# Optimization experiments

Measured on AMD Instinct MI355X. Metric: run time of the kernel, lower is better.

The kernel has to match this reference:

```python
import jax, jax.numpy as jnp
import numpy as np

B, T, H, HW = 16, 32, 512, 32  # batch, timesteps, hidden channels, spatial size


def setup_inputs() -> dict:
    key = jax.random.key(0)
    k1, k2, k3, k4, k5 = jax.random.split(key, 5)
    x = jax.random.normal(k1, (B, T, HW, HW), dtype=jnp.float32)
    # cell conv: 1x1, (1 + H) -> 4H, with bias (k=1 default, padding 'same')
    W_conv = jax.random.normal(k2, (4 * H, 1 + H, 1, 1), dtype=jnp.float32) * 0.02
    b_conv = jax.random.normal(k3, (4 * H,), dtype=jnp.float32) * 0.02
    # post conv: 3x3, H -> 1, padding 'same'
    W_post = jax.random.normal(k4, (1, H, 3, 3), dtype=jnp.float32) * 0.02
    b_post = jax.random.normal(k5, (1,), dtype=jnp.float32) * 0.02
    return {"x": x, "W_conv": W_conv, "b_conv": b_conv, "W_post": W_post, "b_post": b_post}


def _post_conv(h, W_post, b_post):
    # NCHW 3x3 'same' conv
    y = jax.lax.conv_general_dilated(
        h, W_post, window_strides=(1, 1), padding="SAME",
        dimension_numbers=("NCHW", "OIHW", "NCHW"))
    return y + b_post[None, :, None, None]


def reference(x, W_conv, b_conv, W_post, b_post):
    Wc = W_conv[:, :, 0, 0]  # [4H, 1+H] -- 1x1 conv is a channel GEMM

    def step(carry, xt):
        h, c = carry  # [B,H,32,32] each; xt [B,1,32,32]
        z = jnp.concatenate([xt, h], axis=1)  # [B,1+H,32,32]
        gates = jnp.einsum("bchw,oc->bohw", z, Wc) + b_conv[None, :, None, None]
        i, f, o, g = jnp.split(gates, 4, axis=1)
        # Faithful to source (non-standard gating):
        c = jax.nn.sigmoid(f) * c + jax.nn.sigmoid(i) + jnp.tanh(g)
        h = jax.nn.sigmoid(o) + jnp.tanh(c)
        y = _post_conv(h, W_post, b_post)  # [B,1,32,32]
        return (h, c), y

    h0 = jnp.zeros((x.shape[0], H, HW, HW), dtype=x.dtype)
    c0 = jnp.zeros_like(h0)
    xs = x[:, :, None, :, :].transpose(1, 0, 2, 3, 4)  # [T,B,1,32,32]
    _, ys = jax.lax.scan(step, (h0, c0), xs)  # ys [T,B,1,32,32]
    out = ys[:, :, 0].transpose(1, 0, 2, 3)  # [B,T,32,32] == cat along dim=1
    return out
```

## Files before the change

kernel.cpp:

```cpp
#include <hip/hip_runtime.h>
#include <cstdint>
#include <cstddef>

#define B_    16
#define T_    32
#define H_    512
#define P_    1024
#define NPOS  16384
#define NG    2048

typedef __attribute__((ext_vector_type(8))) short short8;
typedef __attribute__((ext_vector_type(4))) float f32x4;

__device__ __forceinline__ unsigned short f2bf(float f) {
  uint32_t u = __float_as_uint(f);
  u += 0x7fffu + ((u >> 16) & 1u);
  return (unsigned short)(u >> 16);
}
__device__ __forceinline__ float bflo(uint32_t u) { return __uint_as_float(u << 16); }
__device__ __forceinline__ float bfhi(uint32_t u) { return __uint_as_float(u & 0xffff0000u); }

__device__ __forceinline__ float sigf(float x) {
  return __builtin_amdgcn_rcpf(1.0f + __expf(-x));
}
__device__ __forceinline__ float tanhf_(float x) {
  return 1.0f - 2.0f * __builtin_amdgcn_rcpf(__expf(2.0f * x) + 1.0f);
}

__device__ __forceinline__ void gload_lds16(const void* g, void* l) {
  __builtin_amdgcn_global_load_lds(
      (const __attribute__((address_space(1))) void*)g,
      (__attribute__((address_space(3))) void*)l, 16, 0, 0);
}

__global__ void repack_w(const float* __restrict__ Wc, const float* __restrict__ bconv,
                         unsigned short* __restrict__ Wp, float* __restrict__ w0x,
                         float* __restrict__ bx) {
  int idx = blockIdx.x * 256 + threadIdx.x;
  int r = idx >> 9, k = idx & 511;
  int ch = r >> 2, g = r & 3;
  int o = g * 512 + ch;
  Wp[idx] = f2bf(Wc[o * 513 + 1 + k]);
  if (k == 0) { w0x[r] = Wc[o * 513]; bx[r] = bconv[o]; }
}

__global__ void repack_wpost(const float* __restrict__ Wpost, float* __restrict__ wpp) {
  int idx = blockIdx.x * 256 + threadIdx.x;
  if (idx >= 9 * 512) return;
  int j = idx >> 9, c = idx & 511;
  wpp[idx] = Wpost[c * 9 + j];
}

__global__ __launch_bounds__(256, 2)
void lstm_step(const unsigned short* __restrict__ Wp,
               const unsigned short* __restrict__ hprev,
               unsigned short* __restrict__ hnext,
               _Float16* __restrict__ Cst,
               const float* __restrict__ w0x, const float* __restrict__ bxv,
               const float* __restrict__ xin, int t) {
  __shared__ unsigned short As[256 * 64];
  __shared__ unsigned short Bs[128 * 64];

  const int tid = threadIdx.x;
  const int lane = tid & 63;
  const int wv = tid >> 6;
  const int wm = wv >> 1, wn = wv & 1;
  const int q = lane >> 4, l = lane & 15;

  const int lid = blockIdx.x;
  const int xcd = lid & 7;
  const int s   = lid >> 3;
  const int ny  = xcd * 16 + (s & 15);
  const int rx  = s >> 4;
  const int r0  = rx * 256;
  const int n0  = ny * 128;
  const int ch0 = rx * 64;

  const int srow = tid >> 3;
  const int lchunk = (tid & 7) ^ (srow & 7);
  const unsigned short* gA = Wp    + (size_t)(r0 + srow) * 512 + lchunk * 8;
  const unsigned short* gB = hprev + (size_t)(n0 + srow) * 512 + lchunk * 8;
  char* lA = (char*)As + wv * 1024;
  char* lB = (char*)Bs + wv * 1024;

  f32x4 acc[8][4] = {};

  for (int kc = 0; kc < 512; kc += 64) {
#pragma unroll
    for (int j = 0; j < 8; ++j)
      gload_lds16(gA + (size_t)j * (32 * 512) + kc, lA + j * 4096);
#pragma unroll
    for (int j = 0; j < 4; ++j)
      gload_lds16(gB + (size_t)j * (32 * 512) + kc, lB + j * 4096);
    __syncthreads();

#pragma unroll
    for (int kk = 0; kk < 2; ++kk) {
      short8 af[8], bf_[4];
#pragma unroll
      for (int mi = 0; mi < 8; ++mi) {
        int row = wm * 128 + mi * 16 + l;
        int sidx = row * 64 + (((kk * 4 + q) ^ (row & 7)) * 8);
        af[mi] = *(const short8*)(As + sidx);
      }
#pragma unroll
      for (int ni = 0; ni < 4; ++ni) {
        int row = wn * 64 + ni * 16 + l;
        int sidx = row * 64 + (((kk * 4 + q) ^ (row & 7)) * 8);
        bf_[ni] = *(const short8*)(Bs + sidx);
      }
#pragma unroll
      for (int mi = 0; mi < 8; ++mi)
#pragma unroll
        for (int ni = 0; ni < 4; ++ni)
          acc[mi][ni] = __builtin_amdgcn_mfma_f32_16x16x32_bf16(af[mi], bf_[ni], acc[mi][ni], 0, 0, 0);
    }
    __syncthreads();
  }

  float xv[4]; int posL[4]; size_t cbase[4];
#pragma unroll
  for (int ni = 0; ni < 4; ++ni) {
    posL[ni] = wn * 64 + ni * 16 + l;
    int pos = n0 + posL[ni];
    int b = pos >> 10, p = pos & 1023;
    xv[ni] = xin[((b * T_ + t) << 10) + p];
    cbase[ni] = ((size_t)b << 19) + p;
  }
#pragma unroll
  for (int mi = 0; mi < 8; ++mi) {
    int chl = wm * 32 + mi * 4 + q;
    int rg = r0 + wm * 128 + mi * 16 + q * 4;
    float4 w0 = *(const float4*)(w0x + rg);
    float4 bb = *(const float4*)(bxv + rg);
    int ch = ch0 + chl;
#pragma unroll
    for (int ni = 0; ni < 4; ++ni) {
      f32x4 g = acc[mi][ni];
      float gi = g[0] + w0.x * xv[ni] + bb.x;
      float gf = g[1] + w0.y * xv[ni] + bb.y;
      float go = g[2] + w0.z * xv[ni] + bb.z;
      float gg = g[3] + w0.w * xv[ni] + bb.w;
      size_t cidx = cbase[ni] + ((size_t)ch << 10);
      float cold = (float)Cst[cidx];
      float cn = sigf(gf) * cold + sigf(gi) + tanhf_(gg);
      float hn = sigf(go) + tanhf_(cn);
      Cst[cidx] = (_Float16)cn;
      As[posL[ni] * 64 + (chl ^ ((posL[ni] & 7) << 3))] = f2bf(hn);
    }
  }
  __syncthreads();
  {
    int pl = tid >> 1;
    int cb = (tid & 1) << 2;
    const unsigned short* srcrow = As + pl * 64;
    unsigned short* dst = hnext + (size_t)(n0 + pl) * 512 + ch0 + (cb << 3);
#pragma unroll
    for (int i = 0; i < 4; ++i)
      ((uint4*)dst)[i] = *(const uint4*)(srcrow + (((cb + i) ^ (pl & 7)) << 3));
  }
}

__global__ __launch_bounds__(256)
void conv_u(const unsigned short* __restrict__ h, const float* __restrict__ wpp,
            float* __restrict__ u) {
  int wid = blockIdx.x * 4 + (threadIdx.x >> 6);
  int lane = threadIdx.x & 63;
  int c0 = lane << 3;
  const uint4 hv = *(const uint4*)(h + ((size_t)wid << 9) + c0);
  float hc0 = bflo(hv.x), hc1 = bfhi(hv.x), hc2 = bflo(hv.y), hc3 = bfhi(hv.y);
  float hc4 = bflo(hv.z), hc5 = bfhi(hv.z), hc6 = bflo(hv.w), hc7 = bfhi(hv.w);
  int b = wid >> 10, p = wid & 1023;
  float outv = 0.f;
#pragma unroll
  for (int j = 0; j < 9; ++j) {
    const float4 wa = *(const float4*)(wpp + (j << 9) + c0);
    const float4 wb = *(const float4*)(wpp + (j << 9) + c0 + 4);
    float a = hc0 * wa.x + hc1 * wa.y + hc2 * wa.z + hc3 * wa.w
            + hc4 * wb.x + hc5 * wb.y + hc6 * wb.z + hc7 * wb.w;
#pragma unroll
    for (int off = 1; off < 64; off <<= 1)
      a += __shfl_xor(a, off, 64);
    if (lane == j) outv = a;
  }
  if (lane < 9)
    u[((b * 9 + lane) << 10) + p] = outv;
}

__global__ __launch_bounds__(256)
void conv_st(const float* __restrict__ u, const float* __restrict__ bpost,
             float* __restrict__ out, int t) {
  int idx = blockIdx.x * 256 + threadIdx.x;
  int b = idx >> 10, p = idx & 1023;
  int py = p >> 5, px = p & 31;
  float acc = bpost[0];
#pragma unroll
  for (int dy = -1; dy <= 1; ++dy) {
    int ny = py + dy;
    if ((unsigned)ny > 31u) continue;
#pragma unroll
    for (int dx = -1; dx <= 1; ++dx) {
      int nx = px + dx;
      if ((unsigned)nx > 31u) continue;
      int j = (dy + 1) * 3 + (dx + 1);
      acc += u[((b * 9 + j) << 10) + (ny << 5) + nx];
    }
  }
  out[((b * T_ + t) << 10) + p] = acc;
}

extern "C" void kernel_launch(void* const* d_in, const int* in_sizes, int n_in,
                              void* d_out, int out_size, void* d_ws, size_t ws_size,
                              hipStream_t stream) {
  const float* x     = (const float*)d_in[0];
  const float* Wconv = (const float*)d_in[1];
  const float* bconv = (const float*)d_in[2];
  const float* Wpost = (const float*)d_in[3];
  const float* bpost = (const float*)d_in[4];
  float* out = (float*)d_out;
  char* ws = (char*)d_ws;

  unsigned short* h0  = (unsigned short*)(ws);
  unsigned short* h1  = (unsigned short*)(ws + 16777216);
  _Float16*       Cst = (_Float16*)(ws + 33554432);
  unsigned short* Wp  = (unsigned short*)(ws + 50331648);
  float*          w0x = (float*)(ws + 52428800);
  float*          bx  = (float*)(ws + 52436992);
  float*          wpp = (float*)(ws + 52445184);
  float*          u   = (float*)(ws + 52463616);

  hipMemsetAsync(h0, 0, 16777216, stream);
  hipMemsetAsync(Cst, 0, 16777216, stream);
  repack_w<<<4096, 256, 0, stream>>>(Wconv, bconv, Wp, w0x, bx);
  repack_wpost<<<18, 256, 0, stream>>>(Wpost, wpp);

  unsigned short* hp = h0;
  unsigned short* hn = h1;
  for (int t = 0; t < T_; ++t) {
    lstm_step<<<1024, 256, 0, stream>>>(Wp, hp, hn, Cst, w0x, bx, x, t);
    conv_u<<<4096, 256, 0, stream>>>(hn, wpp, u);
    conv_st<<<64, 256, 0, stream>>>(u, bpost, out, t);
    unsigned short* tmp = hp; hp = hn; hn = tmp;
  }
}
```

Baseline: 1.975 ms.

## Fuse post-conv channel reduction into LSTM step epilogue via split-bf16 MFMA

Removes the separate conv_u kernel. Each LSTM block now contracts its 64-channel slice of h with the 3x3 post-conv weights inside its epilogue, using MFMA on the h tile already in LDS. The weights are split into hi and lo bf16 parts to keep close to fp32 accuracy. Each block writes per-channel-group partial sums, and conv_st2 adds the 8 partials together with the spatial stencil. This avoids re-reading h from global memory and one launch per timestep, at the cost of extra MFMA work in the epilogue and 8x more partial-sum traffic in the stencil kernel.

```diff
diff --git a/kernel.cpp b/kernel.cpp
--- a/kernel.cpp
+++ b/kernel.cpp
@@ -44,11 +44,15 @@
   if (k == 0) { w0x[r] = Wc[o * 513]; bx[r] = bconv[o]; }
 }
 
-__global__ void repack_wpost(const float* __restrict__ Wpost, float* __restrict__ wpp) {
+__global__ void repack_wpost(const float* __restrict__ Wpost, unsigned short* __restrict__ wppb) {
   int idx = blockIdx.x * 256 + threadIdx.x;
-  if (idx >= 9 * 512) return;
+  if (idx >= 16 * 512) return;
   int j = idx >> 9, c = idx & 511;
-  wpp[idx] = Wpost[c * 9 + j];
+  float v = (j < 9) ? Wpost[c * 9 + j] : 0.f;
+  unsigned short hi = f2bf(v);
+  float lo = v - bflo((uint32_t)hi);
+  wppb[idx] = hi;
+  wppb[16 * 512 + idx] = f2bf(lo);
 }
 
 __global__ __launch_bounds__(256, 2)
@@ -57,7 +61,9 @@
                unsigned short* __restrict__ hnext,
                _Float16* __restrict__ Cst,
                const float* __restrict__ w0x, const float* __restrict__ bxv,
-               const float* __restrict__ xin, int t) {
+               const float* __restrict__ xin,
+               const unsigned short* __restrict__ wppb,
+               float* __restrict__ up, int t) {
   __shared__ unsigned short As[256 * 64];
   __shared__ unsigned short Bs[128 * 64];
 
@@ -150,46 +156,52 @@
     }
   }
   __syncthreads();
+
   {
     int pl = tid >> 1;
-    int cb = (tid & 1) << 2;
+    int cb2 = (tid & 1) << 2;
     const unsigned short* srcrow = As + pl * 64;
-    unsigned short* dst = hnext + (size_t)(n0 + pl) * 512 + ch0 + (cb << 3);
+    unsigned short* dst = hnext + (size_t)(n0 + pl) * 512 + ch0 + (cb2 << 3);
 #pragma unroll
     for (int i = 0; i < 4; ++i)
-      ((uint4*)dst)[i] = *(const uint4*)(srcrow + (((cb + i) ^ (pl & 7)) << 3));
+      ((uint4*)dst)[i] = *(const uint4*)(srcrow + (((cb2 + i) ^ (pl & 7)) << 3));
+  }
+
+  {
+    const unsigned short* wb_hi = wppb;
+    const unsigned short* wb_lo = wppb + 16 * 512;
+    const int posg = wv * 32;
+    f32x4 a2[2] = {};
+#pragma unroll
+    for (int kk = 0; kk < 2; ++kk) {
+      const int wo = l * 512 + ch0 + kk * 32 + q * 8;
+      short8 whi = *(const short8*)(wb_hi + wo);
+      short8 wlo = *(const short8*)(wb_lo + wo);
+#pragma unroll
+      for (int ni2 = 0; ni2 < 2; ++ni2) {
+        int row = posg + ni2 * 16 + l;
+        int sidx = row * 64 + (((kk * 4 + q) ^ (row & 7)) * 8);
+        short8 hf = *(const short8*)(As + sidx);
+        a2[ni2] = __builtin_amdgcn_mfma_f32_16x16x32_bf16(whi, hf, a2[ni2], 0, 0, 0);
+        a2[ni2] = __builtin_amdgcn_mfma_f32_16x16x32_bf16(wlo, hf, a2[ni2], 0, 0, 0);
+      }
+    }
+#pragma unroll
+    for (int ni2 = 0; ni2 < 2; ++ni2) {
+      int pix = n0 + posg + ni2 * 16 + l;
+#pragma unroll
+      for (int r = 0; r < 4; ++r) {
+        int j = q * 4 + r;
+        if (j < 9)
+          up[(size_t)(rx * 9 + j) * NPOS + pix] = a2[ni2][r];
+      }
+    }
   }
 }
 
 __global__ __launch_bounds__(256)
-void conv_u(const unsigned short* __restrict__ h, const float* __restrict__ wpp,
-            float* __restrict__ u) {
-  int wid = blockIdx.x * 4 + (threadIdx.x >> 6);
-  int lane = threadIdx.x & 63;
-  int c0 = lane << 3;
-  const uint4 hv = *(const uint4*)(h + ((size_t)wid << 9) + c0);
-  float hc0 = bflo(hv.x), hc1 = bfhi(hv.x), hc2 = bflo(hv.y), hc3 = bfhi(hv.y);
-  float hc4 = bflo(hv.z), hc5 = bfhi(hv.z), hc6 = bflo(hv.w), hc7 = bfhi(hv.w);
-  int b = wid >> 10, p = wid & 1023;
-  float outv = 0.f;
-#pragma unroll
-  for (int j = 0; j < 9; ++j) {
-    const float4 wa = *(const float4*)(wpp + (j << 9) + c0);
-    const float4 wb = *(const float4*)(wpp + (j << 9) + c0 + 4);
-    float a = hc0 * wa.x + hc1 * wa.y + hc2 * wa.z + hc3 * wa.w
-            + hc4 * wb.x + hc5 * wb.y + hc6 * wb.z + hc7 * wb.w;
-#pragma unroll
-    for (int off = 1; off < 64; off <<= 1)
-      a += __shfl_xor(a, off, 64);
-    if (lane == j) outv = a;
-  }
-  if (lane < 9)
-    u[((b * 9 + lane) << 10) + p] = outv;
-}
-
-__global__ __launch_bounds__(256)
-void conv_st(const float* __restrict__ u, const float* __restrict__ bpost,
-             float* __restrict__ out, int t) {
+void conv_st2(const float* __restrict__ up, const float* __restrict__ bpost,
+              float* __restrict__ out, int t) {
   int idx = blockIdx.x * 256 + threadIdx.x;
   int b = idx >> 10, p = idx & 1023;
   int py = p >> 5, px = p & 31;
@@ -203,7 +215,10 @@
       int nx = px + dx;
       if ((unsigned)nx > 31u) continue;
       int j = (dy + 1) * 3 + (dx + 1);
-      acc += u[((b * 9 + j) << 10) + (ny << 5) + nx];
+      int np = (b << 10) + (ny << 5) + nx;
+#pragma unroll
+      for (int rx = 0; rx < 8; ++rx)
+        acc += up[(size_t)(rx * 9 + j) * NPOS + np];
     }
   }
   out[((b * T_ + t) << 10) + p] = acc;
@@ -220,26 +235,25 @@
   float* out = (float*)d_out;
   char* ws = (char*)d_ws;
 
-  unsigned short* h0  = (unsigned short*)(ws);
-  unsigned short* h1  = (unsigned short*)(ws + 16777216);
-  _Float16*       Cst = (_Float16*)(ws + 33554432);
-  unsigned short* Wp  = (unsigned short*)(ws + 50331648);
-  float*          w0x = (float*)(ws + 52428800);
-  float*          bx  = (float*)(ws + 52436992);
-  float*          wpp = (float*)(ws + 52445184);
-  float*          u   = (float*)(ws + 52463616);
+  unsigned short* h0   = (unsigned short*)(ws);
+  unsigned short* h1   = (unsigned short*)(ws + 16777216);
+  _Float16*       Cst  = (_Float16*)(ws + 33554432);
+  unsigned short* Wp   = (unsigned short*)(ws + 50331648);
+  float*          w0x  = (float*)(ws + 52428800);
+  float*          bx   = (float*)(ws + 52436992);
+  unsigned short* wppb = (unsigned short*)(ws + 52445184);
+  float*          up   = (float*)(ws + 52477952);
 
   hipMemsetAsync(h0, 0, 16777216, stream);
   hipMemsetAsync(Cst, 0, 16777216, stream);
   repack_w<<<4096, 256, 0, stream>>>(Wconv, bconv, Wp, w0x, bx);
-  repack_wpost<<<18, 256, 0, stream>>>(Wpost, wpp);
+  repack_wpost<<<32, 256, 0, stream>>>(Wpost, wppb);
 
   unsigned short* hp = h0;
   unsigned short* hn = h1;
   for (int t = 0; t < T_; ++t) {
-    lstm_step<<<1024, 256, 0, stream>>>(Wp, hp, hn, Cst, w0x, bx, x, t);
-    conv_u<<<4096, 256, 0, stream>>>(hn, wpp, u);
-    conv_st<<<64, 256, 0, stream>>>(u, bpost, out, t);
+    lstm_step<<<1024, 256, 0, stream>>>(Wp, hp, hn, Cst, w0x, bx, x, wppb, up, t);
+    conv_st2<<<64, 256, 0, stream>>>(up, bpost, out, t);
     unsigned short* tmp = hp; hp = hn; hn = tmp;
   }
 }
```

Result: faster. 1.763 ms (-10.7%).
